# Kernel optimization log

Hardware: AMD Instinct MI355X
Metric: run time of the kernel (lower is better)

## Reference

```python
import jax, jax.numpy as jnp
import numpy as np

N_NODES = 100000
N_EDGES = 1000000
F_IN = 64
HIDDEN = 128
BN_EPS = 1e-5
COS_EPS = 1e-8


def setup_inputs() -> dict:
    key = jax.random.key(0)
    ks = jax.random.split(key, 8)
    x = jax.random.normal(ks[0], (N_NODES, F_IN), dtype=jnp.float32)
    edge_index = jax.random.randint(ks[1], (2, N_EDGES), 0, N_NODES, dtype=jnp.int64)
    W1 = jax.random.normal(ks[2], (F_IN, HIDDEN), dtype=jnp.float32) / np.sqrt(F_IN)
    b1 = jax.random.normal(ks[3], (HIDDEN,), dtype=jnp.float32) * 0.01
    gamma = jnp.ones((HIDDEN,), dtype=jnp.float32)
    beta = jnp.zeros((HIDDEN,), dtype=jnp.float32)
    W2 = jax.random.normal(ks[4], (HIDDEN, HIDDEN), dtype=jnp.float32) / np.sqrt(HIDDEN)
    b2 = jax.random.normal(ks[5], (HIDDEN,), dtype=jnp.float32) * 0.01
    return {"x": x, "edge_index": edge_index, "W1": W1, "b1": b1,
            "gamma": gamma, "beta": beta, "W2": W2, "b2": b2}


def _parser(e, W1, b1, gamma, beta, W2, b2):
    # e: (E, F_IN) -> (E, HIDDEN). Linear -> ReLU -> BatchNorm1d (batch stats) -> [Dropout=identity] -> Linear
    h = jnp.maximum(e @ W1 + b1, 0.0)
    mu = jnp.mean(h, axis=0)
    var = jnp.mean(jnp.square(h - mu), axis=0)  # biased variance, as BN uses
    h = (h - mu) * jax.lax.rsqrt(var + BN_EPS) * gamma + beta
    return h @ W2 + b2


def reference(x, edge_index, W1, b1, gamma, beta, W2, b2):
    # Per-edge node feature gather (standard PAE semantics)
    x1 = x[edge_index[0]]  # (E, F_IN)
    x2 = x[edge_index[1]]  # (E, F_IN)
    h1 = _parser(x1, W1, b1, gamma, beta, W2, b2)
    h2 = _parser(x2, W1, b1, gamma, beta, W2, b2)
    dot = jnp.sum(h1 * h2, axis=-1)
    n1 = jnp.sqrt(jnp.sum(jnp.square(h1), axis=-1))
    n2 = jnp.sqrt(jnp.sum(jnp.square(h2), axis=-1))
    cos = dot / jnp.maximum(n1 * n2, COS_EPS)
    return (cos + 1.0) * 0.5  # (E,)
```

## Files before the change

### kernel.cpp

```cpp
#include <hip/hip_runtime.h>
#include <math.h>

#define N_NODES 100000
#define N_PAD   100032
#define N_EDGES 1000000
#define F_IN 64
#define HID 128
#define C2 256
#define ZT 1563
#define ZGRID 256
#define FB 64
#define YGRID 512
#define RANGES 4
#define RSIZE 25000
#define BPR 50
#define EPB (N_EDGES / BPR)

typedef unsigned int uint32;
typedef __bf16 bf16x8 __attribute__((ext_vector_type(8)));
typedef float f32x4 __attribute__((ext_vector_type(4)));
typedef unsigned short ushort8v __attribute__((ext_vector_type(8)));

__device__ __forceinline__ unsigned short bf_top(float f) {
  union { float f; uint32 u; } c; c.f = f;
  c.u = c.u + 0x7fffu + ((c.u >> 16) & 1u);
  return (unsigned short)(c.u >> 16);
}
__device__ __forceinline__ float bf_round(float f) {
  union { float f; uint32 u; } c; c.f = f;
  c.u = (c.u + 0x7fffu + ((c.u >> 16) & 1u)) & 0xffff0000u;
  return c.f;
}
__device__ __forceinline__ float bf_lo(uint32 u) {
  union { uint32 u; float f; } c; c.u = u << 16; return c.f;
}
__device__ __forceinline__ float bf_hi(uint32 u) {
  union { uint32 u; float f; } c; c.u = u & 0xffff0000u; return c.f;
}

__global__ __launch_bounds__(1024) void hist_kernel(const int* __restrict__ ei,
                                                    uint32* __restrict__ Part) {
  __shared__ uint32 h[RSIZE];
  int range = blockIdx.x / BPR, blk = blockIdx.x % BPR;
  int lo = range * RSIZE, hi = lo + RSIZE;
  for (int i = threadIdx.x; i < RSIZE; i += 1024) h[i] = 0;
  __syncthreads();
  int e0 = blk * EPB;
  for (int e = e0 + threadIdx.x; e < e0 + EPB; e += 1024) {
    int i = ei[e], j = ei[N_EDGES + e];
    if (i >= lo && i < hi) atomicAdd(&h[i - lo], 1u);
    if (j >= lo && j < hi) atomicAdd(&h[j - lo], 0x10000u);
  }
  __syncthreads();
  uint32* p = Part + (size_t)blockIdx.x * RSIZE;
  for (int i = threadIdx.x; i < RSIZE; i += 1024) p[i] = h[i];
}

__global__ __launch_bounds__(256) void creduce_kernel(const uint32* __restrict__ Part,
                                                      float* __restrict__ c0f,
                                                      float* __restrict__ c1f) {
  int n = blockIdx.x * 256 + threadIdx.x;
  if (n >= N_NODES) return;
  int range = n / RSIZE, i = n - range * RSIZE;
  const uint32* p = Part + (size_t)range * BPR * RSIZE + i;
  uint32 s = 0;
#pragma unroll 10
  for (int b = 0; b < BPR; ++b) s += p[(size_t)b * RSIZE];
  c0f[n] = (float)(s & 0xffffu);
  c1f[n] = (float)(s >> 16);
}

__global__ __launch_bounds__(256) void zpass_kernel(const float* __restrict__ x,
                                                    const float* __restrict__ W1,
                                                    const float* __restrict__ b1,
                                                    const float* __restrict__ c0f,
                                                    const float* __restrict__ c1f,
                                                    uint4* __restrict__ Zfrag,
                                                    float* __restrict__ Spart) {
  __shared__ __align__(16) unsigned short zstage[8192];
  float* red = (float*)zstage;
  int tid = threadIdx.x;
  int l = tid & 63, w = tid >> 6;
  int lr = l & 15, lg = l >> 4;
  bf16x8 Bf[8][2];
  float b1v[8];
#pragma unroll
  for (int cb = 0; cb < 8; ++cb) {
    int col = cb * 16 + lr;
    b1v[cb] = b1[col];
#pragma unroll
    for (int kc = 0; kc < 2; ++kc) {
      union { ushort8v u; bf16x8 b; } cv;
#pragma unroll
      for (int j = 0; j < 8; ++j) cv.u[j] = bf_top(W1[(kc * 32 + lg * 8 + j) * HID + col]);
      Bf[cb][kc] = cv.b;
    }
  }
  float s10[8] = {}, s20[8] = {}, s11[8] = {}, s21[8] = {};
  for (int t = blockIdx.x; t < ZT; t += ZGRID) {
    int nbase = t * 64;
    int row = nbase + w * 16 + lr;
    bool ok = row < N_NODES;
    bf16x8 A[2];
#pragma unroll
    for (int kc = 0; kc < 2; ++kc) {
      float4 x0 = make_float4(0.f, 0.f, 0.f, 0.f), x1 = x0;
      if (ok) {
        x0 = *(const float4*)&x[(size_t)row * F_IN + kc * 32 + lg * 8];
        x1 = *(const float4*)&x[(size_t)row * F_IN + kc * 32 + lg * 8 + 4];
      }
      union { ushort8v u; bf16x8 b; } cv;
      cv.u[0] = bf_top(x0.x); cv.u[1] = bf_top(x0.y); cv.u[2] = bf_top(x0.z); cv.u[3] = bf_top(x0.w);
      cv.u[4] = bf_top(x1.x); cv.u[5] = bf_top(x1.y); cv.u[6] = bf_top(x1.z); cv.u[7] = bf_top(x1.w);
      A[kc] = cv.b;
    }
    float cc0[4], cc1[4];
#pragma unroll
    for (int r = 0; r < 4; ++r) {
      int node = nbase + w * 16 + lg * 4 + r;
      bool okr = node < N_NODES;
      cc0[r] = okr ? c0f[node] : 0.f;
      cc1[r] = okr ? c1f[node] : 0.f;
    }
    __syncthreads();
#pragma unroll
    for (int cb = 0; cb < 8; ++cb) {
      f32x4 acc = {0.f, 0.f, 0.f, 0.f};
      acc = __builtin_amdgcn_mfma_f32_16x16x32_bf16(A[0], Bf[cb][0], acc, 0, 0, 0);
      acc = __builtin_amdgcn_mfma_f32_16x16x32_bf16(A[1], Bf[cb][1], acc, 0, 0, 0);
      int ks = cb >> 1;
      int lamb = ((cb & 1) * 2 + (lr >> 3)) * 16;
#pragma unroll
      for (int r = 0; r < 4; ++r) {
        float z = fmaxf(acc[r] + b1v[cb], 0.f);
        s10[cb] = fmaf(cc0[r], z, s10[cb]);
        s20[cb] = fmaf(cc0[r] * z, z, s20[cb]);
        s11[cb] = fmaf(cc1[r], z, s11[cb]);
        s21[cb] = fmaf(cc1[r] * z, z, s21[cb]);
        int zi = (w * 4 + ks) * 512 + (lamb + lg * 4 + r) * 8 + (lr & 7);
        zi ^= ((zi >> 7) & 1) << 4;
        zstage[zi] = bf_top(z);
      }
    }
    __syncthreads();
    const uint4* zs4 = (const uint4*)zstage;
    for (int i = tid; i < 1024; i += 256) {
      int si = i ^ (((i >> 4) & 1) << 1);
      Zfrag[(size_t)t * 1024 + i] = zs4[si];
    }
  }
  __syncthreads();
#pragma unroll
  for (int cb = 0; cb < 8; ++cb) {
    float a = s10[cb]; a += __shfl_xor(a, 16); a += __shfl_xor(a, 32);
    float b = s20[cb]; b += __shfl_xor(b, 16); b += __shfl_xor(b, 32);
    float c = s11[cb]; c += __shfl_xor(c, 16); c += __shfl_xor(c, 32);
    float d = s21[cb]; d += __shfl_xor(d, 16); d += __shfl_xor(d, 32);
    if (lg == 0) {
      int feat = cb * 16 + lr;
      red[(w * 4 + 0) * 128 + feat] = a;
      red[(w * 4 + 1) * 128 + feat] = b;
      red[(w * 4 + 2) * 128 + feat] = c;
      red[(w * 4 + 3) * 128 + feat] = d;
    }
  }
  __syncthreads();
  for (int o = tid; o < 512; o += 256) {
    int stat = o >> 7, feat = o & 127;
    float s = red[(0 * 4 + stat) * 128 + feat] + red[(1 * 4 + stat) * 128 + feat] +
              red[(2 * 4 + stat) * 128 + feat] + red[(3 * 4 + stat) * 128 + feat];
    Spart[(size_t)blockIdx.x * 512 + o] = s;
  }
}

__global__ __launch_bounds__(512) void finalize_a(const float* __restrict__ Spart,
                                                  float* __restrict__ S2) {
  int t = threadIdx.x, b = blockIdx.x;
  float s = 0.f;
  for (int p = b; p < ZGRID; p += FB) s += Spart[(size_t)p * 512 + t];
  S2[(size_t)b * 512 + t] = s;
}

__global__ __launch_bounds__(512) void finalize_b(const float* __restrict__ S2,
                                                  const float* __restrict__ gamma,
                                                  const float* __restrict__ beta,
                                                  const float* __restrict__ W2,
                                                  const float* __restrict__ b2,
                                                  float* __restrict__ q,
                                                  unsigned short* __restrict__ Wct) {
  __shared__ float S[512];
  __shared__ float sh[256];
  __shared__ float scs[256];
  int t = threadIdx.x;
  float s = 0.f;
  for (int b = 0; b < FB; ++b) s += S2[(size_t)b * 512 + t];
  S[t] = s;
  __syncthreads();
  if (t < 128) {
    const float invE = 1.0f / (float)N_EDGES;
    float mu0 = S[t] * invE;
    float v0 = fmaxf(S[128 + t] * invE - mu0 * mu0, 0.f);
    float sc0 = gamma[t] * rsqrtf(v0 + 1e-5f);
    scs[t] = sc0;
    sh[t] = beta[t] - mu0 * sc0;
    float mu1 = S[256 + t] * invE;
    float v1 = fmaxf(S[384 + t] * invE - mu1 * mu1, 0.f);
    float sc1 = gamma[t] * rsqrtf(v1 + 1e-5f);
    scs[128 + t] = sc1;
    sh[128 + t] = beta[t] - mu1 * sc1;
  }
  __syncthreads();
  if (t < 256) {
    int side = t >> 7, c = t & 127;
    float acc = b2[c];
    for (int ff = 0; ff < HID; ++ff) acc = fmaf(sh[side * 128 + ff], W2[ff * HID + c], acc);
    q[t] = acc;
  }
  for (int i = t; i < C2 * HID; i += 512) {
    int col = i >> 7, k = i & 127;
    int side = col >> 7, c = col & 127;
    float v = W2[k * HID + c] * scs[side * 128 + k];
    Wct[(col * HID + k) ^ ((col & 7) << 3)] = bf_top(v);
  }
}

__global__ __launch_bounds__(512, 4) void ygemm_kernel(const uint4* __restrict__ Zfrag,
                                                       const unsigned short* __restrict__ Wct,
                                                       const float* __restrict__ q,
                                                       unsigned short* __restrict__ Yb,
                                                       float* __restrict__ n1o,
                                                       float* __restrict__ n2o) {
  __shared__ __align__(16) unsigned short wcs[C2 * HID];
  __shared__ float nrm2[2][256];
  int tid = threadIdx.x;
  {
    const uint4* src = (const uint4*)Wct;
    uint4* dst = (uint4*)wcs;
    for (int c = tid; c < C2 * HID / 8; c += 512) dst[c] = src[c];
  }
  __syncthreads();
  int l = tid & 63, w = tid >> 6;
  int lr = l & 15, lg = l >> 4;
  int rg = w & 1, cg = w >> 1;
  bf16x8 Bf[4][4];
  float qv[4];
#pragma unroll
  for (int cb = 0; cb < 4; ++cb) {
    int col = (cg * 4 + cb) * 16 + lr;
    qv[cb] = q[col];
#pragma unroll
    for (int ks = 0; ks < 4; ++ks) {
      int idx = (col * HID + ks * 32 + lg * 8) ^ ((col & 7) << 3);
      Bf[cb][ks] = *(const bf16x8*)&wcs[idx];
    }
  }
  int p = 0;
  for (int t = blockIdx.x; t < ZT; t += YGRID, p ^= 1) {
    int nbase = t * 64;
    f32x4 acc[2][4] = {};
#pragma unroll
    for (int ks = 0; ks < 4; ++ks) {
      union { uint4 u; bf16x8 b; } A0, A1;
      A0.u = Zfrag[((size_t)t * 16 + rg * 8 + ks) * 64 + l];
      A1.u = Zfrag[((size_t)t * 16 + rg * 8 + 4 + ks) * 64 + l];
#pragma unroll
      for (int cb = 0; cb < 4; ++cb) {
        acc[0][cb] = __builtin_amdgcn_mfma_f32_16x16x32_bf16(A0.b, Bf[cb][ks], acc[0][cb], 0, 0, 0);
        acc[1][cb] = __builtin_amdgcn_mfma_f32_16x16x32_bf16(A1.b, Bf[cb][ks], acc[1][cb], 0, 0, 0);
      }
    }
    float sq[2][4] = {{0.f, 0.f, 0.f, 0.f}, {0.f, 0.f, 0.f, 0.f}};
#pragma unroll
    for (int nh = 0; nh < 2; ++nh) {
#pragma unroll
      for (int cb = 0; cb < 4; ++cb) {
        int col = (cg * 4 + cb) * 16 + lr;
#pragma unroll
        for (int r = 0; r < 4; ++r) {
          float y = bf_round(acc[nh][cb][r] + qv[cb]);
          sq[nh][r] += y * y;
          int grow = nbase + rg * 32 + nh * 16 + lg * 4 + r;
          if (grow < N_NODES) Yb[(size_t)grow * C2 + col] = bf_top(y);
        }
      }
    }
#pragma unroll
    for (int nh = 0; nh < 2; ++nh)
#pragma unroll
      for (int r = 0; r < 4; ++r) {
        float s = sq[nh][r];
        s += __shfl_xor(s, 1); s += __shfl_xor(s, 2);
        s += __shfl_xor(s, 4); s += __shfl_xor(s, 8);
        sq[nh][r] = s;
      }
    if (lr == 0) {
#pragma unroll
      for (int nh = 0; nh < 2; ++nh)
#pragma unroll
        for (int r = 0; r < 4; ++r)
          nrm2[p][w * 32 + nh * 16 + lg * 4 + r] = sq[nh][r];
    }
    __syncthreads();
    if (tid < 64) {
      int row = tid, rg2 = row >> 5, rl = row & 31, grow = nbase + row;
      if (grow < N_NODES) {
        n1o[grow] = sqrtf(nrm2[p][rg2 * 32 + rl] + nrm2[p][(2 + rg2) * 32 + rl]);
        n2o[grow] = sqrtf(nrm2[p][(4 + rg2) * 32 + rl] + nrm2[p][(6 + rg2) * 32 + rl]);
      }
    }
  }
}

__device__ __forceinline__ float dp4(uint4 a, uint4 b) {
  return bf_lo(a.x) * bf_lo(b.x) + bf_hi(a.x) * bf_hi(b.x) +
         bf_lo(a.y) * bf_lo(b.y) + bf_hi(a.y) * bf_hi(b.y) +
         bf_lo(a.z) * bf_lo(b.z) + bf_hi(a.z) * bf_hi(b.z) +
         bf_lo(a.w) * bf_lo(b.w) + bf_hi(a.w) * bf_hi(b.w);
}

__global__ __launch_bounds__(256) void edge_kernel(const int* __restrict__ ei,
                                                   const unsigned short* __restrict__ Yb,
                                                   const float* __restrict__ n1,
                                                   const float* __restrict__ n2,
                                                   float* __restrict__ out) {
  int tid = blockIdx.x * blockDim.x + threadIdx.x;
  int g = tid >> 3, ls = tid & 7;
  int ng = (gridDim.x * blockDim.x) >> 3;
  const uint32* Yw = (const uint32*)Yb;
  for (int e = g; e < N_EDGES; e += 2 * ng) {
    int e2 = e + ng;
    bool h2 = e2 < N_EDGES;
    int i1 = ei[e], j1 = ei[N_EDGES + e];
    int i2 = h2 ? ei[e2] : i1, j2 = h2 ? ei[N_EDGES + e2] : j1;
    const uint4* pa1 = (const uint4*)(Yw + (size_t)i1 * 128 + ls * 8);
    const uint4* pb1 = (const uint4*)(Yw + (size_t)j1 * 128 + 64 + ls * 8);
    const uint4* pa2 = (const uint4*)(Yw + (size_t)i2 * 128 + ls * 8);
    const uint4* pb2 = (const uint4*)(Yw + (size_t)j2 * 128 + 64 + ls * 8);
    uint4 a10 = pa1[0], a11 = pa1[1], b10 = pb1[0], b11 = pb1[1];
    uint4 a20 = pa2[0], a21 = pa2[1], b20 = pb2[0], b21 = pb2[1];
    float d1 = dp4(a10, b10) + dp4(a11, b11);
    float d2 = dp4(a20, b20) + dp4(a21, b21);
    d1 += __shfl_xor(d1, 1); d1 += __shfl_xor(d1, 2); d1 += __shfl_xor(d1, 4);
    d2 += __shfl_xor(d2, 1); d2 += __shfl_xor(d2, 2); d2 += __shfl_xor(d2, 4);
    if (ls == 0) {
      out[e] = (d1 / fmaxf(n1[i1] * n2[j1], 1e-8f) + 1.0f) * 0.5f;
      if (h2) out[e2] = (d2 / fmaxf(n1[i2] * n2[j2], 1e-8f) + 1.0f) * 0.5f;
    }
  }
}

extern "C" void kernel_launch(void* const* d_in, const int* in_sizes, int n_in,
                              void* d_out, int out_size, void* d_ws, size_t ws_size,
                              hipStream_t stream) {
  const float* x = (const float*)d_in[0];
  const int* ei = (const int*)d_in[1];
  const float* W1 = (const float*)d_in[2];
  const float* b1 = (const float*)d_in[3];
  const float* gamma = (const float*)d_in[4];
  const float* beta = (const float*)d_in[5];
  const float* W2 = (const float*)d_in[6];
  const float* b2 = (const float*)d_in[7];
  float* out = (float*)d_out;

  auto align = [](size_t v) { return (v + 255) & ~(size_t)255; };
  char* ws = (char*)d_ws;
  size_t o_part = 0;
  size_t o_c0 = o_part + align((size_t)RANGES * BPR * RSIZE * sizeof(uint32));
  size_t o_c1 = o_c0 + align(N_NODES * sizeof(float));
  size_t o_sp = o_c1 + align(N_NODES * sizeof(float));
  size_t o_s2 = o_sp + align((size_t)ZGRID * 512 * sizeof(float));
  size_t o_q = o_s2 + align((size_t)FB * 512 * sizeof(float));
  size_t o_wct = o_q + align(C2 * sizeof(float));
  size_t o_n1 = o_wct + align((size_t)C2 * HID * sizeof(unsigned short));
  size_t o_n2 = o_n1 + align(N_NODES * sizeof(float));
  size_t o_Z = o_n2 + align(N_NODES * sizeof(float));
  size_t o_Y = o_Z + align((size_t)ZT * 1024 * sizeof(uint4));

  uint32* Part = (uint32*)(ws + o_part);
  float* c0f = (float*)(ws + o_c0);
  float* c1f = (float*)(ws + o_c1);
  float* Sp = (float*)(ws + o_sp);
  float* S2 = (float*)(ws + o_s2);
  float* q = (float*)(ws + o_q);
  unsigned short* Wct = (unsigned short*)(ws + o_wct);
  float* n1 = (float*)(ws + o_n1);
  float* n2 = (float*)(ws + o_n2);
  uint4* Zfrag = (uint4*)(ws + o_Z);
  unsigned short* Yb = (unsigned short*)(ws + o_Y);

  hist_kernel<<<RANGES * BPR, 1024, 0, stream>>>(ei, Part);
  creduce_kernel<<<(N_NODES + 255) / 256, 256, 0, stream>>>(Part, c0f, c1f);
  zpass_kernel<<<ZGRID, 256, 0, stream>>>(x, W1, b1, c0f, c1f, Zfrag, Sp);
  finalize_a<<<FB, 512, 0, stream>>>(Sp, S2);
  finalize_b<<<1, 512, 0, stream>>>(S2, gamma, beta, W2, b2, q, Wct);
  ygemm_kernel<<<YGRID, 512, 0, stream>>>(Zfrag, Wct, q, Yb, n1, n2);
  edge_kernel<<<2048, 256, 0, stream>>>(ei, Yb, n1, n2, out);
}
```

Baseline: 168.4 us.

## Quantize per-node projected features to int8 and use sdot4 for edge cosines

The GEMM epilogue now quantizes each node's 128-wide projected vector per side to int8, with a per-row absmax scale, instead of storing bf16. It stores the reciprocal integer norm so the edge kernel computes the cosine from an integer sdot4 dot product times two gathered scalars. This halves the bytes gathered per edge in the random-access edge pass and the Y write, and adds register prefetch of the next Z tile in the GEMM. The cost is int8 quantization error on the cosine output, an extra block barrier per tile, and dropping the occupancy hint from launch bounds.

```diff
diff --git a/kernel.cpp b/kernel.cpp
--- a/kernel.cpp
+++ b/kernel.cpp
@@ -2,7 +2,6 @@
 #include <math.h>
 
 #define N_NODES 100000
-#define N_PAD   100032
 #define N_EDGES 1000000
 #define F_IN 64
 #define HID 128
@@ -26,17 +25,21 @@
   c.u = c.u + 0x7fffu + ((c.u >> 16) & 1u);
   return (unsigned short)(c.u >> 16);
 }
-__device__ __forceinline__ float bf_round(float f) {
-  union { float f; uint32 u; } c; c.f = f;
-  c.u = (c.u + 0x7fffu + ((c.u >> 16) & 1u)) & 0xffff0000u;
-  return c.f;
-}
-__device__ __forceinline__ float bf_lo(uint32 u) {
-  union { uint32 u; float f; } c; c.u = u << 16; return c.f;
-}
-__device__ __forceinline__ float bf_hi(uint32 u) {
-  union { uint32 u; float f; } c; c.u = u & 0xffff0000u; return c.f;
-}
+
+#if defined(__has_builtin)
+#if __has_builtin(__builtin_amdgcn_sdot4)
+#define SDOT4(a, b, c) __builtin_amdgcn_sdot4((int)(a), (int)(b), (c), false)
+#endif
+#endif
+#ifndef SDOT4
+__device__ __forceinline__ int sdot4_sw(uint32 a, uint32 b, int c) {
+#pragma unroll
+  for (int k = 0; k < 4; ++k)
+    c += (int)(signed char)(a >> (8 * k)) * (int)(signed char)(b >> (8 * k));
+  return c;
+}
+#define SDOT4(a, b, c) sdot4_sw(a, b, c)
+#endif
 
 __global__ __launch_bounds__(1024) void hist_kernel(const int* __restrict__ ei,
                                                     uint32* __restrict__ Part) {
@@ -224,14 +227,15 @@
   }
 }
 
-__global__ __launch_bounds__(512, 4) void ygemm_kernel(const uint4* __restrict__ Zfrag,
-                                                       const unsigned short* __restrict__ Wct,
-                                                       const float* __restrict__ q,
-                                                       unsigned short* __restrict__ Yb,
-                                                       float* __restrict__ n1o,
-                                                       float* __restrict__ n2o) {
+__global__ __launch_bounds__(512) void ygemm_kernel(const uint4* __restrict__ Zfrag,
+                                                    const unsigned short* __restrict__ Wct,
+                                                    const float* __restrict__ q,
+                                                    uint32* __restrict__ Yq,
+                                                    float* __restrict__ g0o,
+                                                    float* __restrict__ g1o) {
   __shared__ __align__(16) unsigned short wcs[C2 * HID];
-  __shared__ float nrm2[2][256];
+  __shared__ float maxb[256];
+  __shared__ int sqb[256];
   int tid = threadIdx.x;
   {
     const uint4* src = (const uint4*)Wct;
@@ -242,6 +246,7 @@
   int l = tid & 63, w = tid >> 6;
   int lr = l & 15, lg = l >> 4;
   int rg = w & 1, cg = w >> 1;
+  int side = cg >> 1, cgl = cg & 1;
   bf16x8 Bf[4][4];
   float qv[4];
 #pragma unroll
@@ -254,97 +259,136 @@
       Bf[cb][ks] = *(const bf16x8*)&wcs[idx];
     }
   }
-  int p = 0;
-  for (int t = blockIdx.x; t < ZT; t += YGRID, p ^= 1) {
+  int t = blockIdx.x;
+  uint4 Ac[8];
+  if (t < ZT) {
+#pragma unroll
+    for (int u = 0; u < 8; ++u) Ac[u] = Zfrag[((size_t)t * 16 + rg * 8 + u) * 64 + l];
+  }
+  for (; t < ZT; t += YGRID) {
     int nbase = t * 64;
+    int tn = t + YGRID;
+    uint4 An[8];
+    if (tn < ZT) {
+#pragma unroll
+      for (int u = 0; u < 8; ++u) An[u] = Zfrag[((size_t)tn * 16 + rg * 8 + u) * 64 + l];
+    }
     f32x4 acc[2][4] = {};
 #pragma unroll
     for (int ks = 0; ks < 4; ++ks) {
       union { uint4 u; bf16x8 b; } A0, A1;
-      A0.u = Zfrag[((size_t)t * 16 + rg * 8 + ks) * 64 + l];
-      A1.u = Zfrag[((size_t)t * 16 + rg * 8 + 4 + ks) * 64 + l];
+      A0.u = Ac[ks];
+      A1.u = Ac[4 + ks];
 #pragma unroll
       for (int cb = 0; cb < 4; ++cb) {
         acc[0][cb] = __builtin_amdgcn_mfma_f32_16x16x32_bf16(A0.b, Bf[cb][ks], acc[0][cb], 0, 0, 0);
         acc[1][cb] = __builtin_amdgcn_mfma_f32_16x16x32_bf16(A1.b, Bf[cb][ks], acc[1][cb], 0, 0, 0);
       }
     }
-    float sq[2][4] = {{0.f, 0.f, 0.f, 0.f}, {0.f, 0.f, 0.f, 0.f}};
-#pragma unroll
-    for (int nh = 0; nh < 2; ++nh) {
-#pragma unroll
-      for (int cb = 0; cb < 4; ++cb) {
-        int col = (cg * 4 + cb) * 16 + lr;
-#pragma unroll
-        for (int r = 0; r < 4; ++r) {
-          float y = bf_round(acc[nh][cb][r] + qv[cb]);
-          sq[nh][r] += y * y;
-          int grow = nbase + rg * 32 + nh * 16 + lg * 4 + r;
-          if (grow < N_NODES) Yb[(size_t)grow * C2 + col] = bf_top(y);
+    float ym[2][4];
+#pragma unroll
+    for (int nh = 0; nh < 2; ++nh)
+#pragma unroll
+      for (int r = 0; r < 4; ++r) {
+        float m = 0.f;
+#pragma unroll
+        for (int cb = 0; cb < 4; ++cb) {
+          float y = acc[nh][cb][r] + qv[cb];
+          acc[nh][cb][r] = y;
+          m = fmaxf(m, fabsf(y));
         }
-      }
-    }
+#pragma unroll
+        for (int s = 1; s <= 8; s <<= 1) m = fmaxf(m, __shfl_xor(m, s));
+        ym[nh][r] = m;
+      }
+    if (lr == 0) {
+#pragma unroll
+      for (int nh = 0; nh < 2; ++nh)
+#pragma unroll
+        for (int r = 0; r < 4; ++r) maxb[w * 32 + nh * 16 + lg * 4 + r] = ym[nh][r];
+    }
+    __syncthreads();
+    int sqi[2][4];
+    uint32 qpack[2][4];
 #pragma unroll
     for (int nh = 0; nh < 2; ++nh)
 #pragma unroll
       for (int r = 0; r < 4; ++r) {
-        float s = sq[nh][r];
-        s += __shfl_xor(s, 1); s += __shfl_xor(s, 2);
-        s += __shfl_xor(s, 4); s += __shfl_xor(s, 8);
-        sq[nh][r] = s;
+        int ro = nh * 16 + lg * 4 + r;
+        float cmax = fmaxf(maxb[(side * 4 + rg) * 32 + ro], maxb[(side * 4 + rg + 2) * 32 + ro]);
+        float inv = cmax > 0.f ? 127.f / cmax : 0.f;
+        int ssum = 0;
+        uint32 pk = 0;
+#pragma unroll
+        for (int cb = 0; cb < 4; ++cb) {
+          int qi = (int)rintf(acc[nh][cb][r] * inv);
+          ssum += qi * qi;
+          pk |= ((uint32)(qi & 0xff)) << (8 * cb);
+        }
+        sqi[nh][r] = ssum;
+        qpack[nh][r] = pk;
+      }
+#pragma unroll
+    for (int nh = 0; nh < 2; ++nh)
+#pragma unroll
+      for (int r = 0; r < 4; ++r) {
+        int grow = nbase + rg * 32 + nh * 16 + lg * 4 + r;
+        if (grow < N_NODES)
+          Yq[(size_t)grow * 64 + side * 32 + cgl * 16 + lr] = qpack[nh][r];
+      }
+#pragma unroll
+    for (int nh = 0; nh < 2; ++nh)
+#pragma unroll
+      for (int r = 0; r < 4; ++r) {
+        int s = sqi[nh][r];
+#pragma unroll
+        for (int m = 1; m <= 8; m <<= 1) s += __shfl_xor(s, m);
+        sqi[nh][r] = s;
       }
     if (lr == 0) {
 #pragma unroll
       for (int nh = 0; nh < 2; ++nh)
 #pragma unroll
-        for (int r = 0; r < 4; ++r)
-          nrm2[p][w * 32 + nh * 16 + lg * 4 + r] = sq[nh][r];
+        for (int r = 0; r < 4; ++r) sqb[w * 32 + nh * 16 + lg * 4 + r] = sqi[nh][r];
     }
     __syncthreads();
-    if (tid < 64) {
-      int row = tid, rg2 = row >> 5, rl = row & 31, grow = nbase + row;
+    if (tid < 128) {
+      int sd = tid >> 6, row = tid & 63;
+      int rg2 = row >> 5, ro = row & 31;
+      int sum = sqb[(sd * 4 + rg2) * 32 + ro] + sqb[(sd * 4 + rg2 + 2) * 32 + ro];
+      int grow = nbase + row;
       if (grow < N_NODES) {
-        n1o[grow] = sqrtf(nrm2[p][rg2 * 32 + rl] + nrm2[p][(2 + rg2) * 32 + rl]);
-        n2o[grow] = sqrtf(nrm2[p][(4 + rg2) * 32 + rl] + nrm2[p][(6 + rg2) * 32 + rl]);
-      }
-    }
-  }
-}
-
-__device__ __forceinline__ float dp4(uint4 a, uint4 b) {
-  return bf_lo(a.x) * bf_lo(b.x) + bf_hi(a.x) * bf_hi(b.x) +
-         bf_lo(a.y) * bf_lo(b.y) + bf_hi(a.y) * bf_hi(b.y) +
-         bf_lo(a.z) * bf_lo(b.z) + bf_hi(a.z) * bf_hi(b.z) +
-         bf_lo(a.w) * bf_lo(b.w) + bf_hi(a.w) * bf_hi(b.w);
+        float g = sum > 0 ? rsqrtf((float)sum) : 0.f;
+        (sd ? g1o : g0o)[grow] = g;
+      }
+    }
+#pragma unroll
+    for (int u = 0; u < 8; ++u) Ac[u] = An[u];
+  }
 }
 
 __global__ __launch_bounds__(256) void edge_kernel(const int* __restrict__ ei,
-                                                   const unsigned short* __restrict__ Yb,
-                                                   const float* __restrict__ n1,
-                                                   const float* __restrict__ n2,
+                                                   const uint32* __restrict__ Yq,
+                                                   const float* __restrict__ g0,
+                                                   const float* __restrict__ g1,
                                                    float* __restrict__ out) {
   int tid = blockIdx.x * blockDim.x + threadIdx.x;
   int g = tid >> 3, ls = tid & 7;
   int ng = (gridDim.x * blockDim.x) >> 3;
-  const uint32* Yw = (const uint32*)Yb;
-  for (int e = g; e < N_EDGES; e += 2 * ng) {
-    int e2 = e + ng;
-    bool h2 = e2 < N_EDGES;
-    int i1 = ei[e], j1 = ei[N_EDGES + e];
-    int i2 = h2 ? ei[e2] : i1, j2 = h2 ? ei[N_EDGES + e2] : j1;
-    const uint4* pa1 = (const uint4*)(Yw + (size_t)i1 * 128 + ls * 8);
-    const uint4* pb1 = (const uint4*)(Yw + (size_t)j1 * 128 + 64 + ls * 8);
-    const uint4* pa2 = (const uint4*)(Yw + (size_t)i2 * 128 + ls * 8);
-    const uint4* pb2 = (const uint4*)(Yw + (size_t)j2 * 128 + 64 + ls * 8);
-    uint4 a10 = pa1[0], a11 = pa1[1], b10 = pb1[0], b11 = pb1[1];
-    uint4 a20 = pa2[0], a21 = pa2[1], b20 = pb2[0], b21 = pb2[1];
-    float d1 = dp4(a10, b10) + dp4(a11, b11);
-    float d2 = dp4(a20, b20) + dp4(a21, b21);
-    d1 += __shfl_xor(d1, 1); d1 += __shfl_xor(d1, 2); d1 += __shfl_xor(d1, 4);
-    d2 += __shfl_xor(d2, 1); d2 += __shfl_xor(d2, 2); d2 += __shfl_xor(d2, 4);
+  for (int e = g; e < N_EDGES; e += ng) {
+    int i = ei[e], j = ei[N_EDGES + e];
+    uint4 a = *(const uint4*)(Yq + (size_t)i * 64 + ls * 4);
+    uint4 b = *(const uint4*)(Yq + (size_t)j * 64 + 32 + ls * 4);
+    int d = 0;
+    d = SDOT4(a.x, b.x, d);
+    d = SDOT4(a.y, b.y, d);
+    d = SDOT4(a.z, b.z, d);
+    d = SDOT4(a.w, b.w, d);
+    d += __shfl_xor(d, 1);
+    d += __shfl_xor(d, 2);
+    d += __shfl_xor(d, 4);
     if (ls == 0) {
-      out[e] = (d1 / fmaxf(n1[i1] * n2[j1], 1e-8f) + 1.0f) * 0.5f;
-      if (h2) out[e2] = (d2 / fmaxf(n1[i2] * n2[j2], 1e-8f) + 1.0f) * 0.5f;
+      out[e] = fmaf((float)d * g0[i] * g1[j], 0.5f, 0.5f);
     }
   }
 }
@@ -371,9 +415,9 @@
   size_t o_s2 = o_sp + align((size_t)ZGRID * 512 * sizeof(float));
   size_t o_q = o_s2 + align((size_t)FB * 512 * sizeof(float));
   size_t o_wct = o_q + align(C2 * sizeof(float));
-  size_t o_n1 = o_wct + align((size_t)C2 * HID * sizeof(unsigned short));
-  size_t o_n2 = o_n1 + align(N_NODES * sizeof(float));
-  size_t o_Z = o_n2 + align(N_NODES * sizeof(float));
+  size_t o_g0 = o_wct + align((size_t)C2 * HID * sizeof(unsigned short));
+  size_t o_g1 = o_g0 + align(N_NODES * sizeof(float));
+  size_t o_Z = o_g1 + align(N_NODES * sizeof(float));
   size_t o_Y = o_Z + align((size_t)ZT * 1024 * sizeof(uint4));
 
   uint32* Part = (uint32*)(ws + o_part);
@@ -383,16 +427,16 @@
   float* S2 = (float*)(ws + o_s2);
   float* q = (float*)(ws + o_q);
   unsigned short* Wct = (unsigned short*)(ws + o_wct);
-  float* n1 = (float*)(ws + o_n1);
-  float* n2 = (float*)(ws + o_n2);
+  float* g0 = (float*)(ws + o_g0);
+  float* g1 = (float*)(ws + o_g1);
   uint4* Zfrag = (uint4*)(ws + o_Z);
-  unsigned short* Yb = (unsigned short*)(ws + o_Y);
+  uint32* Yq = (uint32*)(ws + o_Y);
 
   hist_kernel<<<RANGES * BPR, 1024, 0, stream>>>(ei, Part);
   creduce_kernel<<<(N_NODES + 255) / 256, 256, 0, stream>>>(Part, c0f, c1f);
   zpass_kernel<<<ZGRID, 256, 0, stream>>>(x, W1, b1, c0f, c1f, Zfrag, Sp);
   finalize_a<<<FB, 512, 0, stream>>>(Sp, S2);
   finalize_b<<<1, 512, 0, stream>>>(S2, gamma, beta, W2, b2, q, Wct);
-  ygemm_kernel<<<YGRID, 512, 0, stream>>>(Zfrag, Wct, q, Yb, n1, n2);
-  edge_kernel<<<2048, 256, 0, stream>>>(ei, Yb, n1, n2, out);
-}
+  ygemm_kernel<<<YGRID, 512, 0, stream>>>(Zfrag, Wct, q, Yq, g0, g1);
+  edge_kernel<<<2048, 256, 0, stream>>>(ei, Yq, g0, g1, out);
+}
```

Result: faster. 134.9 us (-19.9%).
